# Performance work log

Measured on AMD Instinct MI355X. Metric: run time of the kernel, lower is better.

Reference implementation:

```python
import jax, jax.numpy as jnp
import numpy as np

H = 4096       # hidden_size
NH = 32        # num attention heads
DN = 128       # qk_nope_head_dim
DR = 64        # qk_rope_head_dim
DV = 128       # v_head_dim
QL = 1536      # q_lora_rank
KL = 512       # kv_lora_rank
INH = 32       # indexer heads
IHD = 128      # indexer head_dim (== fp8 quant block -> one scale per head)
TOPK = 512     # index_topk
T = 1024       # prefill tokens
SCALING = (DN + DR) ** -0.5
FP8_MAX = 448.0  # e4m3 max


def _rms(x, w, eps=1e-6):
    return x * jax.lax.rsqrt(jnp.mean(x * x, -1, keepdims=True) + eps) * w


def _ln(x, w, b, eps=1e-6):
    m = jnp.mean(x, -1, keepdims=True)
    v = jnp.mean(jnp.square(x - m), -1, keepdims=True)
    return (x - m) * jax.lax.rsqrt(v + eps) * w + b


def _rope(x, pos):
    # interleaved (non-neox) rotary embedding on the last dim
    d = x.shape[-1]
    inv = 1.0 / (10000.0 ** (jnp.arange(0, d, 2, dtype=jnp.float32) / d))
    ang = pos.astype(jnp.float32)[:, None] * inv  # [T, d/2]
    shape = (x.shape[0],) + (1,) * (x.ndim - 2) + (d // 2,)
    cos = jnp.cos(ang).reshape(shape)
    sin = jnp.sin(ang).reshape(shape)
    x1, x2 = x[..., 0::2], x[..., 1::2]
    return jnp.stack([x1 * cos - x2 * sin, x1 * sin + x2 * cos], -1).reshape(x.shape)


def _forward(hidden_states, w_qkv_a, q_a_ln_w, w_q_b, kv_a_ln_w, w_kv_b, w_o,
             w_idx_qb, w_idx_k, idx_k_ln_w, idx_k_ln_b, w_idx_weights, positions):
    Tq = hidden_states.shape[0]
    neg = jnp.finfo(jnp.float32).min
    # --- fused low-rank QKV-a projection ---
    qkv_a = hidden_states @ w_qkv_a                       # [T, QL+KL+DR]
    q_c, kv_c, k_pe = qkv_a[:, :QL], qkv_a[:, QL:QL + KL], qkv_a[:, QL + KL:]
    q_cn = _rms(q_c, q_a_ln_w)                            # qr (normed q latent)
    # --- MLA decompression ---
    q = (q_cn @ w_q_b).reshape(Tq, NH, DN + DR)
    q_nope, q_pe = q[..., :DN], q[..., DN:]
    kv = (_rms(kv_c, kv_a_ln_w) @ w_kv_b).reshape(Tq, NH, DN + DV)
    k_nope, v = kv[..., :DN], kv[..., DN:]
    q_pe = _rope(q_pe, positions)
    k_pe = _rope(k_pe, positions)                         # [T, DR], shared across heads (MQA)
    # --- lightning indexer (fp8 ue8m0 per-token-group quant emulated in fp32) ---
    qi = (q_cn @ w_idx_qb).reshape(Tq, INH, IHD)
    qi = jnp.concatenate([_rope(qi[..., :DR], positions), qi[..., DR:]], -1)
    ki = _ln(hidden_states @ w_idx_k, idx_k_ln_w, idx_k_ln_b)   # [T, IHD]
    ki = jnp.concatenate([_rope(ki[:, :DR], positions), ki[:, DR:]], -1)
    amax = jnp.max(jnp.abs(qi), -1, keepdims=True)        # group == head (IHD == block 128)
    q_scale = jnp.exp2(jnp.ceil(jnp.log2(jnp.maximum(amax, 1e-10) / FP8_MAX)))  # ue8m0
    qi_q = qi / q_scale                                   # values in fp8 range
    wts = (hidden_states @ w_idx_weights) * q_scale[..., 0]
    wts = wts * (IHD ** -0.5) * (INH ** -0.5)             # [T, INH]
    sim = jax.nn.relu(jnp.einsum('qhd,kd->hqk', qi_q, ki))
    logits = jnp.einsum('qh,hqk->qk', wts, sim)           # [Tq, Tk]
    idx = jnp.arange(Tq)
    causal = idx[:, None] >= idx[None, :]
    logits = jnp.where(causal, logits, neg)
    _, topk_idx = jax.lax.top_k(logits, TOPK)             # [T, TOPK]
    sparse_mask = jnp.zeros((Tq, Tq), bool).at[idx[:, None], topk_idx].set(True) & causal
    # --- sparse MLA attention ---
    qf = jnp.concatenate([q_nope, q_pe], -1)              # [T, NH, DN+DR]
    kf = jnp.concatenate([k_nope, jnp.broadcast_to(k_pe[:, None, :], (Tq, NH, DR))], -1)
    scores = jnp.einsum('qhd,khd->hqk', qf, kf) * SCALING
    scores = jnp.where(sparse_mask[None], scores, neg)
    attn = jax.nn.softmax(scores, -1)
    out = jnp.einsum('hqk,khd->qhd', attn, v).reshape(Tq, NH * DV)
    return out @ w_o                                      # [T, H]


def setup_inputs() -> dict:
    key = jax.random.key(0)
    ks = jax.random.split(key, 8)
    s = 0.02
    return {
        'hidden_states': jax.random.normal(ks[0], (T, H), jnp.float32),
        'positions': jnp.arange(T, dtype=jnp.int32),
        'w_qkv_a': jax.random.normal(ks[1], (H, QL + KL + DR), jnp.float32) * s,
        'q_a_ln_w': jnp.ones((QL,), jnp.float32),
        'w_q_b': jax.random.normal(ks[2], (QL, NH * (DN + DR)), jnp.float32) * s,
        'kv_a_ln_w': jnp.ones((KL,), jnp.float32),
        'w_kv_b': jax.random.normal(ks[3], (KL, NH * (DN + DV)), jnp.float32) * s,
        'w_o': jax.random.normal(ks[4], (NH * DV, H), jnp.float32) * s,
        'w_idx_qb': jax.random.normal(ks[5], (QL, INH * IHD), jnp.float32) * s,
        'w_idx_k': jax.random.normal(ks[6], (H, IHD), jnp.float32) * s,
        'idx_k_ln_w': jnp.ones((IHD,), jnp.float32),
        'idx_k_ln_b': jnp.zeros((IHD,), jnp.float32),
        'w_idx_weights': jax.random.normal(ks[7], (H, INH), jnp.float32) * s,
    }


def reference(hidden_states, positions, w_qkv_a, q_a_ln_w, w_q_b, kv_a_ln_w, w_kv_b, w_o,
              w_idx_qb, w_idx_k, idx_k_ln_w, idx_k_ln_b, w_idx_weights):
    return _forward(hidden_states, w_qkv_a, q_a_ln_w, w_q_b, kv_a_ln_w, w_kv_b, w_o,
                    w_idx_qb, w_idx_k, idx_k_ln_w, idx_k_ln_b, w_idx_weights, positions)
```

## Files before the change

### kernel.cpp

```cpp
#include <hip/hip_runtime.h>
#include <hip/hip_bf16.h>
#include <math.h>
#include <type_traits>

#define TT   1024
#define HH   4096
#define NHH  32
#define DNN  128
#define DRR  64
#define DVV  128
#define QLL  1536
#define KLL  512
#define INHH 32
#define IHDD 128
#define TOPKK 512
#define QKVN 2112

typedef __attribute__((ext_vector_type(8))) short short8;
typedef __attribute__((ext_vector_type(4))) short short4v;
typedef __attribute__((ext_vector_type(4))) float f32x4;

static __device__ __constant__ float kScaling = 0.07216878364870322f;
static __device__ __constant__ float kWtsScale = 0.015625f;

static __device__ __forceinline__ short f2bf(float f) {
  unsigned u = __float_as_uint(f);
  unsigned r = (u + 0x7fffu + ((u >> 16) & 1u)) >> 16;
  return (short)r;
}
static __device__ __forceinline__ float bf2f(short s) {
  return __uint_as_float(((unsigned)(unsigned short)s) << 16);
}
static __device__ __forceinline__ void gl16(const void* g, void* l) {
  __builtin_amdgcn_global_load_lds(
      (const __attribute__((address_space(1))) unsigned int*)g,
      (__attribute__((address_space(3))) unsigned int*)l, 16, 0, 0);
}
static __device__ __forceinline__ int xcd_swz(int n, int nwg) {
  const int q = nwg >> 3, r = nwg & 7;
  const int x = n & 7, i = n >> 3;
  return (x < r ? x * (q + 1) : r * (q + 1) + (x - r) * q) + i;
}

template <typename CT>
__global__ __launch_bounds__(256) void gemm_bf16(const short* __restrict__ A,
                                                 const short* __restrict__ Bt,
                                                 CT* __restrict__ C,
                                                 int M, int N, int K) {
  __shared__ short As[64 * 64];
  __shared__ short Bs[128 * 64];
  int flat = blockIdx.x + gridDim.x * blockIdx.y;
  flat = xcd_swz(flat, gridDim.x * gridDim.y);
  const int byg = flat % gridDim.y;
  const int bxg = flat / gridDim.y;
  const int tid = threadIdx.x;
  const int lane = tid & 63, wv = tid >> 6;
  const int wc = wv * 32;
  const int bm = byg * 64, bn = bxg * 128;
  const int l15 = lane & 15, l4 = lane >> 4;
  const int sx = (l15 & 7) * 8;
  f32x4 acc[4][2];
#pragma unroll
  for (int i = 0; i < 4; ++i)
#pragma unroll
    for (int j = 0; j < 2; ++j) acc[i][j] = f32x4{0.f, 0.f, 0.f, 0.f};
  for (int k0 = 0; k0 < K; k0 += 64) {
    __syncthreads();
#pragma unroll
    for (int i = 0; i < 2; ++i) {
      const int idx = tid + i * 256;
      const int row = idx >> 3, c8 = (idx & 7) * 8;
      const int cs = c8 ^ ((row & 7) * 8);
      gl16(A + (size_t)(bm + row) * K + k0 + cs, &As[idx * 8]);
    }
#pragma unroll
    for (int i = 0; i < 4; ++i) {
      const int idx = tid + i * 256;
      const int row = idx >> 3, c8 = (idx & 7) * 8;
      const int cs = c8 ^ ((row & 7) * 8);
      gl16(Bt + (size_t)(bn + row) * K + k0 + cs, &Bs[idx * 8]);
    }
    __syncthreads();
    short8 fa[4][2], fb[2][2];
#pragma unroll
    for (int rt = 0; rt < 4; ++rt)
#pragma unroll
      for (int kk = 0; kk < 2; ++kk)
        fa[rt][kk] = *(const short8*)(&As[(rt * 16 + l15) * 64 + ((kk * 32 + l4 * 8) ^ sx)]);
#pragma unroll
    for (int ct = 0; ct < 2; ++ct)
#pragma unroll
      for (int kk = 0; kk < 2; ++kk)
        fb[ct][kk] = *(const short8*)(&Bs[(wc + ct * 16 + l15) * 64 + ((kk * 32 + l4 * 8) ^ sx)]);
#pragma unroll
    for (int kk = 0; kk < 2; ++kk)
#pragma unroll
      for (int rt = 0; rt < 4; ++rt)
#pragma unroll
        for (int ct = 0; ct < 2; ++ct)
          acc[rt][ct] = __builtin_amdgcn_mfma_f32_16x16x32_bf16(fa[rt][kk], fb[ct][kk], acc[rt][ct], 0, 0, 0);
  }
#pragma unroll
  for (int rt = 0; rt < 4; ++rt)
#pragma unroll
    for (int ct = 0; ct < 2; ++ct)
#pragma unroll
      for (int r = 0; r < 4; ++r) {
        const int row = bm + rt * 16 + l4 * 4 + r;
        const int col = bn + wc + ct * 16 + l15;
        const float v = acc[rt][ct][r];
        if constexpr (std::is_same<CT, float>::value) C[(size_t)row * N + col] = v;
        else C[(size_t)row * N + col] = __float2bfloat16(v);
      }
}

__global__ __launch_bounds__(256) void gemm1_splitk(const short* __restrict__ A,
                                                    const short* __restrict__ Bt,
                                                    float* __restrict__ part,
                                                    int M, int Np, int K, int kchunk) {
  __shared__ short As[64 * 64];
  __shared__ short Bs[128 * 64];
  int flat = blockIdx.x + gridDim.x * (blockIdx.y + gridDim.y * blockIdx.z);
  flat = xcd_swz(flat, gridDim.x * gridDim.y * gridDim.z);
  const int byg = flat % gridDim.y;
  int tmp = flat / gridDim.y;
  const int bxg = tmp % gridDim.x, bzg = tmp / gridDim.x;
  const int tid = threadIdx.x;
  const int lane = tid & 63, wv = tid >> 6;
  const int wc = wv * 32;
  const int bm = byg * 64, bn = bxg * 128;
  const int kbeg = bzg * kchunk;
  const int l15 = lane & 15, l4 = lane >> 4;
  const int sx = (l15 & 7) * 8;
  f32x4 acc[4][2];
#pragma unroll
  for (int i = 0; i < 4; ++i)
#pragma unroll
    for (int j = 0; j < 2; ++j) acc[i][j] = f32x4{0.f, 0.f, 0.f, 0.f};
  for (int k0 = kbeg; k0 < kbeg + kchunk; k0 += 64) {
    __syncthreads();
#pragma unroll
    for (int i = 0; i < 2; ++i) {
      const int idx = tid + i * 256;
      const int row = idx >> 3, c8 = (idx & 7) * 8;
      const int cs = c8 ^ ((row & 7) * 8);
      gl16(A + (size_t)(bm + row) * K + k0 + cs, &As[idx * 8]);
    }
#pragma unroll
    for (int i = 0; i < 4; ++i) {
      const int idx = tid + i * 256;
      const int row = idx >> 3, c8 = (idx & 7) * 8;
      const int cs = c8 ^ ((row & 7) * 8);
      gl16(Bt + (size_t)(bn + row) * K + k0 + cs, &Bs[idx * 8]);
    }
    __syncthreads();
    short8 fa[4][2], fb[2][2];
#pragma unroll
    for (int rt = 0; rt < 4; ++rt)
#pragma unroll
      for (int kk = 0; kk < 2; ++kk)
        fa[rt][kk] = *(const short8*)(&As[(rt * 16 + l15) * 64 + ((kk * 32 + l4 * 8) ^ sx)]);
#pragma unroll
    for (int ct = 0; ct < 2; ++ct)
#pragma unroll
      for (int kk = 0; kk < 2; ++kk)
        fb[ct][kk] = *(const short8*)(&Bs[(wc + ct * 16 + l15) * 64 + ((kk * 32 + l4 * 8) ^ sx)]);
#pragma unroll
    for (int kk = 0; kk < 2; ++kk)
#pragma unroll
      for (int rt = 0; rt < 4; ++rt)
#pragma unroll
        for (int ct = 0; ct < 2; ++ct)
          acc[rt][ct] = __builtin_amdgcn_mfma_f32_16x16x32_bf16(fa[rt][kk], fb[ct][kk], acc[rt][ct], 0, 0, 0);
  }
  float* dst = part + (size_t)bzg * M * Np;
#pragma unroll
  for (int rt = 0; rt < 4; ++rt)
#pragma unroll
    for (int ct = 0; ct < 2; ++ct)
#pragma unroll
      for (int r = 0; r < 4; ++r)
        dst[(size_t)(bm + rt * 16 + l4 * 4 + r) * Np + bn + wc + ct * 16 + l15] =
            acc[rt][ct][r];
}

__global__ __launch_bounds__(256) void gemm3(const short* __restrict__ Ah,
                                             const short* __restrict__ Al,
                                             const short* __restrict__ Bth,
                                             const short* __restrict__ Btl,
                                             float* __restrict__ part,
                                             int M, int Np, int K, int kchunk) {
  __shared__ short AS[64 * 64], BS[128 * 64];
  int flat = blockIdx.x + gridDim.x * (blockIdx.y + gridDim.y * blockIdx.z);
  flat = xcd_swz(flat, gridDim.x * gridDim.y * gridDim.z);
  const int byg = flat % gridDim.y;
  int tmp = flat / gridDim.y;
  const int bxg = tmp % gridDim.x, bzg = tmp / gridDim.x;
  const int tid = threadIdx.x;
  const int lane = tid & 63, wv = tid >> 6;
  const int wc = wv * 32;
  const int l15 = lane & 15, l4 = lane >> 4;
  const int sx = (l15 & 7) * 8;
  const int bm = byg * 64, bn = bxg * 128;
  const int kbeg = bzg * kchunk;
  f32x4 acc[4][2];
#pragma unroll
  for (int i = 0; i < 4; ++i)
#pragma unroll
    for (int j = 0; j < 2; ++j) acc[i][j] = f32x4{0.f, 0.f, 0.f, 0.f};
  for (int k0 = kbeg; k0 < kbeg + kchunk; k0 += 32) {
    __syncthreads();
#pragma unroll
    for (int i = 0; i < 2; ++i) {
      const int idx = tid + i * 256;
      const int row = idx >> 3, c8 = (idx & 7) * 8;
      const int cs = c8 ^ ((row & 7) * 8);
      const short* srcA = (cs < 32) ? (Ah + (size_t)(bm + row) * K + k0 + cs)
                                    : (Al + (size_t)(bm + row) * K + k0 + (cs - 32));
      gl16(srcA, &AS[idx * 8]);
    }
#pragma unroll
    for (int i = 0; i < 4; ++i) {
      const int idx = tid + i * 256;
      const int row = idx >> 3, c8 = (idx & 7) * 8;
      const int cs = c8 ^ ((row & 7) * 8);
      const short* srcB = (cs < 32) ? (Bth + (size_t)(bn + row) * K + k0 + cs)
                                    : (Btl + (size_t)(bn + row) * K + k0 + (cs - 32));
      gl16(srcB, &BS[idx * 8]);
    }
    __syncthreads();
    short8 fah[4], fal[4], fbh[2], fbl[2];
#pragma unroll
    for (int rt = 0; rt < 4; ++rt) {
      const int row = rt * 16 + l15;
      fah[rt] = *(const short8*)&AS[row * 64 + ((l4 * 8) ^ sx)];
      fal[rt] = *(const short8*)&AS[row * 64 + ((32 + l4 * 8) ^ sx)];
    }
#pragma unroll
    for (int ct = 0; ct < 2; ++ct) {
      const int row = wc + ct * 16 + l15;
      fbh[ct] = *(const short8*)&BS[row * 64 + ((l4 * 8) ^ sx)];
      fbl[ct] = *(const short8*)&BS[row * 64 + ((32 + l4 * 8) ^ sx)];
    }
#pragma unroll
    for (int ct = 0; ct < 2; ++ct)
#pragma unroll
      for (int rt = 0; rt < 4; ++rt) {
        acc[rt][ct] = __builtin_amdgcn_mfma_f32_16x16x32_bf16(fah[rt], fbh[ct], acc[rt][ct], 0, 0, 0);
        acc[rt][ct] = __builtin_amdgcn_mfma_f32_16x16x32_bf16(fah[rt], fbl[ct], acc[rt][ct], 0, 0, 0);
        acc[rt][ct] = __builtin_amdgcn_mfma_f32_16x16x32_bf16(fal[rt], fbh[ct], acc[rt][ct], 0, 0, 0);
      }
  }
  float* dst = part + (size_t)bzg * M * Np;
#pragma unroll
  for (int rt = 0; rt < 4; ++rt)
#pragma unroll
    for (int ct = 0; ct < 2; ++ct)
#pragma unroll
      for (int r = 0; r < 4; ++r)
        dst[(size_t)(bm + rt * 16 + l4 * 4 + r) * Np + bn + wc + ct * 16 + l15] =
            acc[rt][ct][r];
}

__global__ __launch_bounds__(256) void reduce_splitk(const float* __restrict__ part,
                                                     float* __restrict__ C,
                                                     int M, int Np, int Nout, int ldC,
                                                     int ksplit) {
  const int c = blockIdx.x * 256 + threadIdx.x;
  const int m = blockIdx.y;
  if (c >= Nout) return;
  float s = 0.f;
  for (int z = 0; z < ksplit; ++z) s += part[((size_t)z * M + m) * Np + c];
  C[(size_t)m * ldC + c] = s;
}

__global__ __launch_bounds__(256) void qkv_post(const float* __restrict__ qpart,
                                                const float* __restrict__ tpart,
                                                const float* __restrict__ q_ln_w,
                                                const float* __restrict__ kv_ln_w,
                                                const int* __restrict__ pos,
                                                short* __restrict__ qcn_bf,
                                                short* __restrict__ qcn_lo,
                                                short* __restrict__ kvn_bf,
                                                short* __restrict__ kpe_bf) {
  const int t = blockIdx.x, tid = threadIdx.x;
  __shared__ float red[4];
  float qv[6];
  float ss = 0.f;
#pragma unroll
  for (int j = 0; j < 6; ++j) {
    const int c = tid + j * 256;
    float s = 0.f;
#pragma unroll
    for (int z = 0; z < 4; ++z) s += qpart[((size_t)z * TT + t) * QLL + c];
    qv[j] = s;
    ss = fmaf(s, s, ss);
  }
#pragma unroll
  for (int o = 32; o > 0; o >>= 1) ss += __shfl_xor(ss, o);
  if ((tid & 63) == 0) red[tid >> 6] = ss;
  __syncthreads();
  const float rq = rsqrtf((red[0] + red[1] + red[2] + red[3]) / (float)QLL + 1e-6f);
  __syncthreads();
#pragma unroll
  for (int j = 0; j < 6; ++j) {
    const int c = tid + j * 256;
    const float v = qv[j] * rq * q_ln_w[c];
    const short h = f2bf(v);
    qcn_bf[(size_t)t * QLL + c] = h;
    qcn_lo[(size_t)t * QLL + c] = f2bf(v - bf2f(h));
  }
  float kv2[2];
  float ss2 = 0.f;
#pragma unroll
  for (int j = 0; j < 2; ++j) {
    const int c = tid + j * 256;
    float s = 0.f;
#pragma unroll
    for (int z = 0; z < 4; ++z) s += tpart[((size_t)z * TT + t) * 640 + c];
    kv2[j] = s;
    ss2 = fmaf(s, s, ss2);
  }
#pragma unroll
  for (int o = 32; o > 0; o >>= 1) ss2 += __shfl_xor(ss2, o);
  if ((tid & 63) == 0) red[tid >> 6] = ss2;
  __syncthreads();
  const float rkv = rsqrtf((red[0] + red[1] + red[2] + red[3]) / (float)KLL + 1e-6f);
#pragma unroll
  for (int j = 0; j < 2; ++j) {
    const int c = tid + j * 256;
    kvn_bf[(size_t)t * KLL + c] = f2bf(kv2[j] * rkv * kv_ln_w[c]);
  }
  if (tid < 32) {
    float x1 = 0.f, x2 = 0.f;
#pragma unroll
    for (int z = 0; z < 4; ++z) {
      x1 += tpart[((size_t)z * TT + t) * 640 + 512 + 2 * tid];
      x2 += tpart[((size_t)z * TT + t) * 640 + 512 + 2 * tid + 1];
    }
    const float inv = powf(10000.f, -(float)tid * (1.f / 32.f));
    float sn, cs;
    sincosf((float)pos[t] * inv, &sn, &cs);
    kpe_bf[(size_t)t * 64 + 2 * tid]     = f2bf(x1 * cs - x2 * sn);
    kpe_bf[(size_t)t * 64 + 2 * tid + 1] = f2bf(x1 * sn + x2 * cs);
  }
}

__global__ __launch_bounds__(256) void ki_prep2(const float* __restrict__ part,
                                                const float* __restrict__ w,
                                                const float* __restrict__ b,
                                                const int* __restrict__ pos,
                                                short* __restrict__ kih,
                                                short* __restrict__ kil,
                                                float* __restrict__ wtsb) {
  const int t = blockIdx.x, tid = threadIdx.x;
  __shared__ float red[4], red2[4];
  float s = 0.f;
#pragma unroll
  for (int z = 0; z < 8; ++z) s += part[((size_t)z * TT + t) * 256 + tid];
  if (tid >= 128 && tid < 160) wtsb[(size_t)t * 32 + (tid - 128)] = s;
  const float v = (tid < 128) ? s : 0.f;
  float sm = v;
#pragma unroll
  for (int o = 32; o > 0; o >>= 1) sm += __shfl_xor(sm, o);
  if ((tid & 63) == 0) red[tid >> 6] = sm;
  __syncthreads();
  const float m = (red[0] + red[1]) * (1.f / 128.f);
  const float dv = v - m;
  float sq = (tid < 128) ? dv * dv : 0.f;
#pragma unroll
  for (int o = 32; o > 0; o >>= 1) sq += __shfl_xor(sq, o);
  if ((tid & 63) == 0) red2[tid >> 6] = sq;
  __syncthreads();
  const float var = (red2[0] + red2[1]) * (1.f / 128.f);
  if (tid < 128) {
    float x = dv * rsqrtf(var + 1e-6f) * w[tid] + b[tid];
    if (tid < 64) {
      const float part2 = __shfl_xor(x, 1);
      const int pi = tid >> 1;
      const float inv = powf(10000.f, -(float)pi * (1.f / 32.f));
      float sn, cs;
      sincosf((float)pos[t] * inv, &sn, &cs);
      x = (tid & 1) ? (part2 * sn + x * cs) : (x * cs - part2 * sn);
    }
    const short h = f2bf(x);
    kih[(size_t)t * 128 + tid] = h;
    kil[(size_t)t * 128 + tid] = f2bf(x - bf2f(h));
  }
}

__global__ __launch_bounds__(256) void split_cast(const float* __restrict__ in,
                                                  short* __restrict__ hi,
                                                  short* __restrict__ lo, int n4) {
  const int i = blockIdx.x * 256 + threadIdx.x;
  if (i >= n4) return;
  float4 v = *(const float4*)(in + (size_t)i * 4);
  float av[4] = {v.x, v.y, v.z, v.w};
  short4v h, l;
#pragma unroll
  for (int e = 0; e < 4; ++e) {
    h[e] = f2bf(av[e]);
    l[e] = f2bf(av[e] - bf2f(h[e]));
  }
  *(short4v*)(hi + (size_t)i * 4) = h;
  *(short4v*)(lo + (size_t)i * 4) = l;
}

__global__ __launch_bounds__(256) void transpose_cast_g(const float* __restrict__ B,
                                                        short* __restrict__ Bt,
                                                        int K, int ldB, int col0, int Ncols) {
  __shared__ float tile[64][65];
  const int tid = threadIdx.x;
  const int k0 = blockIdx.y * 64, n0 = blockIdx.x * 64;
  const int nl = tid >> 3, kc = (tid & 7) * 8;
  if (n0 >= Ncols) {
    short8 z = {0, 0, 0, 0, 0, 0, 0, 0};
#pragma unroll
    for (int i = 0; i < 2; ++i) {
      const int n = nl + i * 32;
      *(short8*)(Bt + (size_t)(n0 + n) * K + k0 + kc) = z;
    }
    return;
  }
  const int r = tid >> 4, c4 = (tid & 15) * 4;
#pragma unroll
  for (int i = 0; i < 4; ++i) {
    float4 v = *(const float4*)(B + (size_t)(k0 + r + i * 16) * ldB + col0 + n0 + c4);
    tile[r + i * 16][c4 + 0] = v.x;
    tile[r + i * 16][c4 + 1] = v.y;
    tile[r + i * 16][c4 + 2] = v.z;
    tile[r + i * 16][c4 + 3] = v.w;
  }
  __syncthreads();
#pragma unroll
  for (int i = 0; i < 2; ++i) {
    const int n = nl + i * 32;
    short8 o;
#pragma unroll
    for (int e = 0; e < 8; ++e) o[e] = f2bf(tile[kc + e][n]);
    *(short8*)(Bt + (size_t)(n0 + n) * K + k0 + kc) = o;
  }
}

__global__ __launch_bounds__(256) void transpose_split_cast(const float* __restrict__ B,
                                                            short* __restrict__ Bth,
                                                            short* __restrict__ Btl,
                                                            int K, int ldB, int col0,
                                                            int Ncols) {
  __shared__ float tile[64][65];
  const int tid = threadIdx.x;
  const int k0 = blockIdx.y * 64, n0 = blockIdx.x * 64;
  const int nl = tid >> 3, kc = (tid & 7) * 8;
  if (n0 >= Ncols) {
    short8 z = {0, 0, 0, 0, 0, 0, 0, 0};
#pragma unroll
    for (int i = 0; i < 2; ++i) {
      const int n = nl + i * 32;
      *(short8*)(Bth + (size_t)(n0 + n) * K + k0 + kc) = z;
      *(short8*)(Btl + (size_t)(n0 + n) * K + k0 + kc) = z;
    }
    return;
  }
  const int r = tid >> 4, c4 = (tid & 15) * 4;
#pragma unroll
  for (int i = 0; i < 4; ++i) {
    float4 v = make_float4(0.f, 0.f, 0.f, 0.f);
    if (n0 + c4 < Ncols)
      v = *(const float4*)(B + (size_t)(k0 + r + i * 16) * ldB + col0 + n0 + c4);
    tile[r + i * 16][c4 + 0] = v.x;
    tile[r + i * 16][c4 + 1] = v.y;
    tile[r + i * 16][c4 + 2] = v.z;
    tile[r + i * 16][c4 + 3] = v.w;
  }
  __syncthreads();
#pragma unroll
  for (int i = 0; i < 2; ++i) {
    const int n = nl + i * 32;
    short8 oh, ol;
#pragma unroll
    for (int e = 0; e < 8; ++e) {
      const float x = tile[kc + e][n];
      oh[e] = f2bf(x);
      ol[e] = f2bf(x - bf2f(oh[e]));
    }
    *(short8*)(Bth + (size_t)(n0 + n) * K + k0 + kc) = oh;
    *(short8*)(Btl + (size_t)(n0 + n) * K + k0 + kc) = ol;
  }
}

__global__ void q_rope_repack(const short* __restrict__ qbuf,
                              short* __restrict__ qhout,
                              const int* __restrict__ pos) {
  const int q = blockIdx.x, h = blockIdx.y;
  const int p = threadIdx.x;
  const short* s = qbuf + ((size_t)q * 32 + h) * 192;
  short* d = qhout + ((size_t)h * 1024 + q) * 192;
  float x1 = bf2f(s[2 * p]), x2 = bf2f(s[2 * p + 1]);
  if (p >= 64) {
    const int i = p - 64;
    const float inv = powf(10000.f, -(float)i * (1.f / 32.f));
    const float ang = (float)pos[q] * inv;
    float sn, cs;
    sincosf(ang, &sn, &cs);
    const float a = x1 * cs - x2 * sn, b = x1 * sn + x2 * cs;
    x1 = a; x2 = b;
  }
  d[2 * p]     = f2bf(x1);
  d[2 * p + 1] = f2bf(x2);
}

__global__ __launch_bounds__(256) void qi_rope_repack_split(const float* __restrict__ qib,
                                                            const int* __restrict__ pos,
                                                            short* __restrict__ qhh,
                                                            short* __restrict__ qhl) {
  const int qt = blockIdx.x, h = blockIdx.y;
  const int tid = threadIdx.x;
#pragma unroll
  for (int i = 0; i < 8; ++i) {
    const int idx = tid + i * 256;
    const int q = idx >> 5, c = idx & 31;
    float4 v = *(const float4*)(qib + ((size_t)(qt * 64 + q) * 32 + h) * 128 + c * 4);
    float av[4] = {v.x, v.y, v.z, v.w};
    if (c < 16) {
      const int qg = qt * 64 + q;
      const float p = (float)pos[qg];
      float sn0, cs0, sn1, cs1;
      sincosf(p * powf(10000.f, -(float)(c * 2) * (1.f / 32.f)), &sn0, &cs0);
      sincosf(p * powf(10000.f, -(float)(c * 2 + 1) * (1.f / 32.f)), &sn1, &cs1);
      const float a0 = av[0] * cs0 - av[1] * sn0, a1 = av[0] * sn0 + av[1] * cs0;
      const float a2 = av[2] * cs1 - av[3] * sn1, a3 = av[2] * sn1 + av[3] * cs1;
      av[0] = a0; av[1] = a1; av[2] = a2; av[3] = a3;
    }
    short4v hv, lv;
#pragma unroll
    for (int e = 0; e < 4; ++e) {
      hv[e] = f2bf(av[e]);
      lv[e] = f2bf(av[e] - bf2f(hv[e]));
    }
    const size_t off = ((size_t)h * 1024 + qt * 64 + q) * 128 + c * 4;
    *(short4v*)(qhh + off) = hv;
    *(short4v*)(qhl + off) = lv;
  }
}

__global__ __launch_bounds__(256) void kv_repack(const short* __restrict__ kvb,
                                                 const short* __restrict__ kpe,
                                                 short* __restrict__ kfout,
                                                 short* __restrict__ vtout) {
  const int kt = blockIdx.x, h = blockIdx.y;
  const int tid = threadIdx.x;
  const int k0 = kt * 64;
  __shared__ short vtile[64][136];
#pragma unroll
  for (int i = 0; i < 6; ++i) {
    const int idx = tid + i * 256;
    const int row = idx / 24, c = idx - row * 24;
    short8 v = (c < 16) ? *(const short8*)(kvb + ((size_t)(k0 + row) * 32 + h) * 256 + c * 8)
                        : *(const short8*)(kpe + (size_t)(k0 + row) * 64 + (c - 16) * 8);
    *(short8*)(kfout + ((size_t)h * 1024 + k0 + row) * 192 + c * 8) = v;
  }
#pragma unroll
  for (int i = 0; i < 4; ++i) {
    const int idx = tid + i * 256;
    const int row = idx >> 4, c = idx & 15;
    *(short8*)&vtile[row][c * 8] =
        *(const short8*)(kvb + ((size_t)(k0 + row) * 32 + h) * 256 + 128 + c * 8);
  }
  __syncthreads();
#pragma unroll
  for (int i = 0; i < 4; ++i) {
    const int idx = tid + i * 256;
    const int d = idx >> 3, kc = idx & 7;
    short8 o;
#pragma unroll
    for (int e = 0; e < 8; ++e) o[e] = vtile[kc * 8 + e][d];
    *(short8*)(vtout + ((size_t)h * 128 + d) * 1024 + k0 + kc * 8) = o;
  }
}

__global__ __launch_bounds__(256) void logits_mfma(const short* __restrict__ qih,
                                                   const short* __restrict__ qil,
                                                   const short* __restrict__ kih_g,
                                                   const short* __restrict__ kil_g,
                                                   const float* __restrict__ wts,
                                                   float* __restrict__ part) {
  const int bid = xcd_swz(blockIdx.x, gridDim.x);
  int bq = (int)((sqrtf(8.f * bid + 1.f) - 1.f) * 0.5f);
  while ((bq + 1) * (bq + 2) / 2 <= bid) ++bq;
  while (bq * (bq + 1) / 2 > bid) --bq;
  const int bk = bid - bq * (bq + 1) / 2;
  const int g = blockIdx.y;
  __shared__ short kih[64 * 128], kil[64 * 128];
  __shared__ float swts[64][8];
  const int tid = threadIdx.x;
  const int lane = tid & 63, wv = tid >> 6;
  const int wr = (wv >> 1) * 32, wc = (wv & 1) * 32;
  const int l15 = lane & 15, l4 = lane >> 4;
  const int q0 = bq * 64, k0 = bk * 64;
  {
    const int r0 = tid >> 4;
    const int c8 = (tid & 15) * 8;
#pragma unroll
    for (int i = 0; i < 4; ++i) {
      const int row = r0 + i * 16;
      gl16(kih_g + (size_t)(k0 + row) * 128 + c8, &kih[(tid + i * 256) * 8]);
      gl16(kil_g + (size_t)(k0 + row) * 128 + c8, &kil[(tid + i * 256) * 8]);
    }
  }
#pragma unroll
  for (int i = 0; i < 2; ++i) {
    const int idx = tid + i * 256;
    swts[idx >> 3][idx & 7] = wts[(size_t)(q0 + (idx >> 3)) * 32 + g * 8 + (idx & 7)];
  }
  __syncthreads();
  short8 kbh[2][4], kbl[2][4];
#pragma unroll
  for (int ct = 0; ct < 2; ++ct)
#pragma unroll
    for (int ks = 0; ks < 4; ++ks) {
      kbh[ct][ks] = *(const short8*)&kih[(wc + ct * 16 + l15) * 128 + ks * 32 + l4 * 8];
      kbl[ct][ks] = *(const short8*)&kil[(wc + ct * 16 + l15) * 128 + ks * 32 + l4 * 8];
    }
  f32x4 lacc[2][2];
#pragma unroll
  for (int i = 0; i < 2; ++i)
#pragma unroll
    for (int j = 0; j < 2; ++j) lacc[i][j] = f32x4{0.f, 0.f, 0.f, 0.f};
  for (int hh = 0; hh < 8; ++hh) {
    const int h = g * 8 + hh;
    short8 qah[2][4], qal[2][4];
#pragma unroll
    for (int rt = 0; rt < 2; ++rt)
#pragma unroll
      for (int ks = 0; ks < 4; ++ks) {
        const size_t off = ((size_t)h * 1024 + q0 + wr + rt * 16 + l15) * 128 + ks * 32 + l4 * 8;
        qah[rt][ks] = *(const short8*)(qih + off);
        qal[rt][ks] = *(const short8*)(qil + off);
      }
    f32x4 hacc[2][2];
#pragma unroll
    for (int i = 0; i < 2; ++i)
#pragma unroll
      for (int j = 0; j < 2; ++j) hacc[i][j] = f32x4{0.f, 0.f, 0.f, 0.f};
#pragma unroll
    for (int ks = 0; ks < 4; ++ks)
#pragma unroll
      for (int rt = 0; rt < 2; ++rt)
#pragma unroll
        for (int ct = 0; ct < 2; ++ct) {
          hacc[rt][ct] = __builtin_amdgcn_mfma_f32_16x16x32_bf16(qah[rt][ks], kbh[ct][ks], hacc[rt][ct], 0, 0, 0);
          hacc[rt][ct] = __builtin_amdgcn_mfma_f32_16x16x32_bf16(qah[rt][ks], kbl[ct][ks], hacc[rt][ct], 0, 0, 0);
          hacc[rt][ct] = __builtin_amdgcn_mfma_f32_16x16x32_bf16(qal[rt][ks], kbh[ct][ks], hacc[rt][ct], 0, 0, 0);
        }
#pragma unroll
    for (int rt = 0; rt < 2; ++rt)
#pragma unroll
      for (int ct = 0; ct < 2; ++ct)
#pragma unroll
        for (int r = 0; r < 4; ++r) {
          const int row = wr + rt * 16 + l4 * 4 + r;
          const float w = swts[row][hh] * kWtsScale;
          lacc[rt][ct][r] = fmaf(w, fmaxf(hacc[rt][ct][r], 0.f), lacc[rt][ct][r]);
        }
  }
#pragma unroll
  for (int rt = 0; rt < 2; ++rt)
#pragma unroll
    for (int ct = 0; ct < 2; ++ct)
#pragma unroll
      for (int r = 0; r < 4; ++r)
        part[(size_t)g * TT * TT + (size_t)(q0 + wr + rt * 16 + l4 * 4 + r) * TT +
             (k0 + wc + ct * 16 + l15)] = lacc[rt][ct][r];
}

__global__ __launch_bounds__(256) void topk_mask(const float* __restrict__ part,
                                                 unsigned* __restrict__ maskbuf) {
  const int w = threadIdx.x >> 6;
  const int lane = threadIdx.x & 63;
  const int q = blockIdx.x * 4 + w;
  const size_t NN = (size_t)TT * TT;
  __shared__ unsigned long long bl[4][16];
  unsigned v[16];
#pragma unroll
  for (int j = 0; j < 16; ++j) {
    const int k = j * 64 + lane;
    unsigned uv = 0u;
    if (k <= q) {
      const size_t o = (size_t)q * TT + k;
      const float s = part[o] + part[NN + o] + part[2 * NN + o] + part[3 * NN + o];
      unsigned bb = __float_as_uint(s);
      uv = (bb & 0x80000000u) ? ~bb : (bb | 0x80000000u);
    }
    v[j] = uv;
  }
  if (q + 1 <= TOPKK) {
#pragma unroll
    for (int j = 0; j < 16; ++j) {
      const unsigned long long m = __ballot(j * 64 + lane <= q);
      if (lane == 0) bl[w][j] = m;
    }
  } else {
    unsigned lo = 1u, hi = 0xFFFFFFFFu;
    while (lo < hi) {
      const unsigned mid = lo + ((hi - lo) >> 1) + ((hi - lo) & 1u);
      int c = 0;
#pragma unroll
      for (int j = 0; j < 16; ++j) c += __popcll(__ballot(v[j] >= mid));
      if (c >= TOPKK) lo = mid; else hi = mid - 1u;
    }
    const unsigned ustar = lo;
    int nGreater = 0;
#pragma unroll
    for (int j = 0; j < 16; ++j) nGreater += __popcll(__ballot(v[j] > ustar));
    int need = TOPKK - nGreater;
    const unsigned long long lanemask = lane ? (~0ull >> (64 - lane)) : 0ull;
#pragma unroll
    for (int j = 0; j < 16; ++j) {
      const unsigned long long bg = __ballot(v[j] > ustar);
      const unsigned long long be = __ballot(v[j] == ustar);
      const int ce = __popcll(be);
      const int take = need < ce ? need : ce;
      const int rank = __popcll(be & lanemask);
      const bool selme = ((be >> lane) & 1ull) && (rank < take);
      const unsigned long long m = bg | __ballot(selme);
      if (lane == 0) bl[w][j] = m;
      need -= take;
    }
  }
  __builtin_amdgcn_s_waitcnt(0);
  if (lane < 32)
    maskbuf[(size_t)q * 32 + lane] = (unsigned)(bl[w][lane >> 1] >> ((lane & 1) * 32));
}

__global__ __launch_bounds__(256) void attn_mfma(const short* __restrict__ qh,
                                                 const short* __restrict__ kf,
                                                 const short* __restrict__ vt,
                                                 const unsigned* __restrict__ maskbuf,
                                                 short* __restrict__ ao) {
  const int h = blockIdx.x;
  const int yy = blockIdx.y;
  const int qt = (yy < 8) ? (yy * 2) : (31 - yy * 2);
  const int tid = threadIdx.x;
  const int lane = tid & 63, w = tid >> 6;
  const int l15 = lane & 15, l4 = lane >> 4;
  const int q0 = qt * 64;
  __shared__ short kfs[64 * 200];
  __shared__ short vts[128 * 72];
  __shared__ short ps[4][16][72];
  __shared__ unsigned m32s[64][2];
  short8 qf[6];
#pragma unroll
  for (int ks = 0; ks < 6; ++ks)
    qf[ks] = *(const short8*)(qh + ((size_t)h * 1024 + q0 + w * 16 + l15) * 192 + ks * 32 + l4 * 8);
  f32x4 of[8];
#pragma unroll
  for (int dt = 0; dt < 8; ++dt) of[dt] = f32x4{0.f, 0.f, 0.f, 0.f};
  float m[4], l[4];
#pragma unroll
  for (int r = 0; r < 4; ++r) { m[r] = -INFINITY; l[r] = 0.f; }

  for (int kt = 0; kt <= qt; ++kt) {
    const int k0 = kt * 64;
    __syncthreads();
#pragma unroll
    for (int i = 0; i < 6; ++i) {
      const int idx = tid + i * 256;
      const int row = idx / 24, c = idx - row * 24;
      *(short8*)&kfs[row * 200 + c * 8] =
          *(const short8*)(kf + ((size_t)h * 1024 + k0 + row) * 192 + c * 8);
    }
#pragma unroll
    for (int i = 0; i < 4; ++i) {
      const int idx = tid + i * 256;
      const int row = idx >> 3, c = idx & 7;
      *(short8*)&vts[row * 72 + c * 8] =
          *(const short8*)(vt + ((size_t)h * 128 + row) * 1024 + k0 + c * 8);
    }
    if (tid < 128)
      m32s[tid >> 1][tid & 1] = maskbuf[(size_t)(q0 + (tid >> 1)) * 32 + (k0 >> 5) + (tid & 1)];
    __syncthreads();
    f32x4 sacc[4];
#pragma unroll
    for (int j = 0; j < 4; ++j) sacc[j] = f32x4{0.f, 0.f, 0.f, 0.f};
#pragma unroll
    for (int ks = 0; ks < 6; ++ks)
#pragma unroll
      for (int j = 0; j < 4; ++j) {
        short8 kb = *(const short8*)&kfs[(j * 16 + l15) * 200 + ks * 32 + l4 * 8];
        sacc[j] = __builtin_amdgcn_mfma_f32_16x16x32_bf16(qf[ks], kb, sacc[j], 0, 0, 0);
      }
    float tmax[4] = {-INFINITY, -INFINITY, -INFINITY, -INFINITY};
#pragma unroll
    for (int j = 0; j < 4; ++j)
#pragma unroll
      for (int r = 0; r < 4; ++r) {
        const int kcol = j * 16 + l15;
        const unsigned um = m32s[w * 16 + l4 * 4 + r][kcol >> 5];
        float s = sacc[j][r] * kScaling;
        s = ((um >> (kcol & 31)) & 1u) ? s : -INFINITY;
        sacc[j][r] = s;
        tmax[r] = fmaxf(tmax[r], s);
      }
#pragma unroll
    for (int r = 0; r < 4; ++r) {
      tmax[r] = fmaxf(tmax[r], __shfl_xor(tmax[r], 1));
      tmax[r] = fmaxf(tmax[r], __shfl_xor(tmax[r], 2));
      tmax[r] = fmaxf(tmax[r], __shfl_xor(tmax[r], 4));
      tmax[r] = fmaxf(tmax[r], __shfl_xor(tmax[r], 8));
    }
    float f[4];
#pragma unroll
    for (int r = 0; r < 4; ++r) {
      const float mn = fmaxf(m[r], tmax[r]);
      f[r] = __expf(fmaxf(m[r], -1e30f) - fmaxf(mn, -1e30f));
      m[r] = mn;
      l[r] *= f[r];
    }
    float psum[4] = {0.f, 0.f, 0.f, 0.f};
#pragma unroll
    for (int j = 0; j < 4; ++j)
#pragma unroll
      for (int r = 0; r < 4; ++r) {
        const float p = __expf(sacc[j][r] - fmaxf(m[r], -1e30f));
        psum[r] += p;
        ps[w][l4 * 4 + r][j * 16 + l15] = f2bf(p);
      }
#pragma unroll
    for (int r = 0; r < 4; ++r) {
      psum[r] += __shfl_xor(psum[r], 1);
      psum[r] += __shfl_xor(psum[r], 2);
      psum[r] += __shfl_xor(psum[r], 4);
      psum[r] += __shfl_xor(psum[r], 8);
      l[r] += psum[r];
    }
#pragma unroll
    for (int dt = 0; dt < 8; ++dt)
#pragma unroll
      for (int r = 0; r < 4; ++r) of[dt][r] *= f[r];
    short8 pa0 = *(const short8*)&ps[w][l15][l4 * 8];
    short8 pa1 = *(const short8*)&ps[w][l15][32 + l4 * 8];
#pragma unroll
    for (int dt = 0; dt < 8; ++dt) {
      short8 vb0 = *(const short8*)&vts[(dt * 16 + l15) * 72 + l4 * 8];
      short8 vb1 = *(const short8*)&vts[(dt * 16 + l15) * 72 + 32 + l4 * 8];
      of[dt] = __builtin_amdgcn_mfma_f32_16x16x32_bf16(pa0, vb0, of[dt], 0, 0, 0);
      of[dt] = __builtin_amdgcn_mfma_f32_16x16x32_bf16(pa1, vb1, of[dt], 0, 0, 0);
    }
  }
#pragma unroll
  for (int r = 0; r < 4; ++r) {
    const float invl = 1.f / l[r];
#pragma unroll
    for (int dt = 0; dt < 8; ++dt)
      ao[(size_t)(q0 + w * 16 + l4 * 4 + r) * 4096 + h * 128 + dt * 16 + l15] =
          f2bf(of[dt][r] * invl);
  }
}

extern "C" void kernel_launch(void* const* d_in, const int* in_sizes, int n_in,
                              void* d_out, int out_size, void* d_ws, size_t ws_size,
                              hipStream_t stream) {
  const float* hidden     = (const float*)d_in[0];
  const int*   positions  = (const int*)d_in[1];
  const float* w_qkv_a    = (const float*)d_in[2];
  const float* q_a_ln_w   = (const float*)d_in[3];
  const float* w_q_b      = (const float*)d_in[4];
  const float* kv_a_ln_w  = (const float*)d_in[5];
  const float* w_kv_b     = (const float*)d_in[6];
  const float* w_o        = (const float*)d_in[7];
  const float* w_idx_qb   = (const float*)d_in[8];
  const float* w_idx_k    = (const float*)d_in[9];
  const float* idx_k_ln_w = (const float*)d_in[10];
  const float* idx_k_ln_b = (const float*)d_in[11];
  const float* w_idx_w    = (const float*)d_in[12];
  float* out = (float*)d_out;

  float* ws = (float*)d_ws;
  size_t off = 0;
  auto take = [&](size_t n) { float* p = ws + off; off += n; return p; };
  short* qcn_bf  = (short*)take((size_t)TT * QLL / 2);
  short* qcn_lo  = (short*)take((size_t)TT * QLL / 2);
  short* kvn_bf  = (short*)take((size_t)TT * KLL / 2);
  short* qbuf    = (short*)take((size_t)TT * NHH * 192 / 2);
  short* kvbuf   = (short*)take((size_t)TT * NHH * 256 / 2);
  short* kpe_bf  = (short*)take((size_t)TT * 32);
  float* qib     = take((size_t)TT * INHH * IHDD);
  float* wtsb    = take((size_t)TT * INHH);
  short* kih_g   = (short*)take((size_t)TT * IHDD / 2);
  short* kil_g   = (short*)take((size_t)TT * IHDD / 2);
  short* qhb     = (short*)take((size_t)NHH * TT * 192 / 2);
  short* qih_h   = (short*)take((size_t)INHH * TT * 128 / 2);
  short* qih_l   = (short*)take((size_t)INHH * TT * 128 / 2);
  short* kfb     = (short*)take((size_t)NHH * TT * 192 / 2);
  short* vtb     = (short*)take((size_t)NHH * 128 * TT / 2);
  float* part4   = take((size_t)4 * TT * TT);
  unsigned* maskbuf = (unsigned*)take((size_t)TT * 32);
  short* hid_h   = (short*)take((size_t)TT * HH / 2);
  short* hid_l   = (short*)take((size_t)TT * HH / 2);
  short* wqkva_h = (short*)take((size_t)QLL * HH / 2);
  short* wqkva_l = (short*)take((size_t)QLL * HH / 2);
  short* wtail_t = (short*)take((size_t)640 * HH / 2);
  short* wsk_h   = (short*)take((size_t)256 * HH / 2);
  short* wsk_l   = (short*)take((size_t)256 * HH / 2);
  short* widxqb_h = (short*)take((size_t)HH * QLL / 2);
  short* widxqb_l = (short*)take((size_t)HH * QLL / 2);
  short* wqb_t   = (short*)take((size_t)6144 * QLL / 2);
  short* wkvb_t  = (short*)take((size_t)8192 * KLL / 2);
  short* ao   = (short*)part4;
  short* wo_t = hid_h;
  float* skpart = part4;
  float* qkvpart = (float*)vtb;
  float* tailpart = (float*)kvbuf;
  float* idxpart = (float*)qhb;

  const dim3 blk(256);
  split_cast<<<dim3(TT * HH / 4 / 256), blk, 0, stream>>>(hidden, hid_h, hid_l, TT * HH / 4);
  transpose_split_cast<<<dim3(QLL / 64, HH / 64), blk, 0, stream>>>(w_qkv_a, wqkva_h, wqkva_l, HH, QKVN, 0, QLL);
  transpose_cast_g<<<dim3(640 / 64, HH / 64), blk, 0, stream>>>(w_qkv_a, wtail_t, HH, QKVN, QLL, QKVN - QLL);
  transpose_split_cast<<<dim3(HH / 64, QLL / 64), blk, 0, stream>>>(w_idx_qb, widxqb_h, widxqb_l, QLL, HH, 0, HH);
  transpose_split_cast<<<dim3(2, HH / 64), blk, 0, stream>>>(w_idx_k, wsk_h, wsk_l, HH, 128, 0, 128);
  transpose_split_cast<<<dim3(2, HH / 64), blk, 0, stream>>>(w_idx_w, wsk_h + (size_t)128 * HH,
                                                            wsk_l + (size_t)128 * HH, HH, 32, 0, 32);
  transpose_cast_g<<<dim3(6144 / 64, QLL / 64), blk, 0, stream>>>(w_q_b, wqb_t, QLL, 6144, 0, 6144);
  transpose_cast_g<<<dim3(8192 / 64, KLL / 64), blk, 0, stream>>>(w_kv_b, wkvb_t, KLL, 8192, 0, 8192);
  gemm3<<<dim3(2, 16, 8), blk, 0, stream>>>(hid_h, hid_l, wsk_h, wsk_l,
                                            skpart, TT, 256, HH, HH / 8);
  ki_prep2<<<dim3(TT), blk, 0, stream>>>(skpart, idx_k_ln_w, idx_k_ln_b, positions,
                                         kih_g, kil_g, wtsb);
  gemm3<<<dim3(QLL / 128, 16, 4), blk, 0, stream>>>(hid_h, hid_l, wqkva_h, wqkva_l,
                                                    qkvpart, TT, QLL, HH, HH / 4);
  gemm1_splitk<<<dim3(5, 16, 4), blk, 0, stream>>>(hid_h, wtail_t, tailpart, TT, 640, HH, HH / 4);
  qkv_post<<<dim3(TT), blk, 0, stream>>>(qkvpart, tailpart, q_a_ln_w, kv_a_ln_w, positions,
                                         qcn_bf, qcn_lo, kvn_bf, kpe_bf);
  transpose_cast_g<<<dim3(HH / 64, HH / 64), blk, 0, stream>>>(w_o, wo_t, HH, HH, 0, HH);
  gemm3<<<dim3(HH / 128, 16, 2), blk, 0, stream>>>(qcn_bf, qcn_lo, widxqb_h, widxqb_l,
                                                   idxpart, TT, HH, QLL, QLL / 2);
  reduce_splitk<<<dim3(HH / 256, TT), blk, 0, stream>>>(idxpart, qib, TT, HH, HH, HH, 2);
  gemm_bf16<__hip_bfloat16><<<dim3(48, 16), blk, 0, stream>>>(qcn_bf, wqb_t, (__hip_bfloat16*)qbuf, TT, 6144, QLL);
  gemm_bf16<__hip_bfloat16><<<dim3(64, 16), blk, 0, stream>>>(kvn_bf, wkvb_t, (__hip_bfloat16*)kvbuf, TT, 8192, KLL);
  q_rope_repack<<<dim3(TT, NHH), 96, 0, stream>>>(qbuf, qhb, positions);
  qi_rope_repack_split<<<dim3(16, INHH), blk, 0, stream>>>(qib, positions, qih_h, qih_l);
  kv_repack<<<dim3(16, NHH), blk, 0, stream>>>(kvbuf, kpe_bf, kfb, vtb);
  logits_mfma<<<dim3(136, 4), blk, 0, stream>>>(qih_h, qih_l, kih_g, kil_g, wtsb, part4);
  topk_mask<<<dim3(TT / 4), blk, 0, stream>>>(part4, maskbuf);
  attn_mfma<<<dim3(NHH, 16), blk, 0, stream>>>(qhb, kfb, vtb, maskbuf, ao);
  gemm_bf16<float><<<dim3(32, 16), blk, 0, stream>>>(ao, wo_t, out, TT, HH, NHH * DVV);
}
```

Baseline: 506.6 us.

## Fuse RoPE/repack epilogues into q_b and kv_b GEMMs and drop split-K reduce

Adds a q_b GEMM whose epilogue applies rotary embedding and writes the head-major attention query layout directly. It also adds a kv_b GEMM whose epilogue writes K in head-major layout and V transposed via shared memory. The qi RoPE repack now sums the two split-K partial planes itself, so the separate reduce kernel and intermediate buffers are gone. This removes several full round trips through global memory and some launches. In exchange the GEMM epilogues do per-element powf/sincos and narrow scattered stores, and a small kpe_fill kernel is added.

```diff
diff --git a/kernel.cpp b/kernel.cpp
--- a/kernel.cpp
+++ b/kernel.cpp
@@ -112,6 +112,182 @@
         if constexpr (std::is_same<CT, float>::value) C[(size_t)row * N + col] = v;
         else C[(size_t)row * N + col] = __float2bfloat16(v);
       }
+}
+
+__global__ __launch_bounds__(256) void gemm_qb(const short* __restrict__ A,
+                                               const short* __restrict__ Bt,
+                                               const int* __restrict__ pos,
+                                               short* __restrict__ qhb) {
+  const int M = TT, N = 6144, K = QLL;
+  __shared__ short As[64 * 64];
+  __shared__ short Bs[128 * 64];
+  int flat = blockIdx.x + gridDim.x * blockIdx.y;
+  flat = xcd_swz(flat, gridDim.x * gridDim.y);
+  const int byg = flat % gridDim.y;
+  const int bxg = flat / gridDim.y;
+  const int tid = threadIdx.x;
+  const int lane = tid & 63, wv = tid >> 6;
+  const int wc = wv * 32;
+  const int bm = byg * 64, bn = bxg * 128;
+  const int l15 = lane & 15, l4 = lane >> 4;
+  const int sx = (l15 & 7) * 8;
+  f32x4 acc[4][2];
+#pragma unroll
+  for (int i = 0; i < 4; ++i)
+#pragma unroll
+    for (int j = 0; j < 2; ++j) acc[i][j] = f32x4{0.f, 0.f, 0.f, 0.f};
+  for (int k0 = 0; k0 < K; k0 += 64) {
+    __syncthreads();
+#pragma unroll
+    for (int i = 0; i < 2; ++i) {
+      const int idx = tid + i * 256;
+      const int row = idx >> 3, c8 = (idx & 7) * 8;
+      const int cs = c8 ^ ((row & 7) * 8);
+      gl16(A + (size_t)(bm + row) * K + k0 + cs, &As[idx * 8]);
+    }
+#pragma unroll
+    for (int i = 0; i < 4; ++i) {
+      const int idx = tid + i * 256;
+      const int row = idx >> 3, c8 = (idx & 7) * 8;
+      const int cs = c8 ^ ((row & 7) * 8);
+      gl16(Bt + (size_t)(bn + row) * K + k0 + cs, &Bs[idx * 8]);
+    }
+    __syncthreads();
+    short8 fa[4][2], fb[2][2];
+#pragma unroll
+    for (int rt = 0; rt < 4; ++rt)
+#pragma unroll
+      for (int kk = 0; kk < 2; ++kk)
+        fa[rt][kk] = *(const short8*)(&As[(rt * 16 + l15) * 64 + ((kk * 32 + l4 * 8) ^ sx)]);
+#pragma unroll
+    for (int ct = 0; ct < 2; ++ct)
+#pragma unroll
+      for (int kk = 0; kk < 2; ++kk)
+        fb[ct][kk] = *(const short8*)(&Bs[(wc + ct * 16 + l15) * 64 + ((kk * 32 + l4 * 8) ^ sx)]);
+#pragma unroll
+    for (int kk = 0; kk < 2; ++kk)
+#pragma unroll
+      for (int rt = 0; rt < 4; ++rt)
+#pragma unroll
+        for (int ct = 0; ct < 2; ++ct)
+          acc[rt][ct] = __builtin_amdgcn_mfma_f32_16x16x32_bf16(fa[rt][kk], fb[ct][kk], acc[rt][ct], 0, 0, 0);
+  }
+#pragma unroll
+  for (int rt = 0; rt < 4; ++rt)
+#pragma unroll
+    for (int r = 0; r < 4; ++r) {
+      const int row = bm + rt * 16 + l4 * 4 + r;
+      const float p = (float)pos[row];
+#pragma unroll
+      for (int ct = 0; ct < 2; ++ct) {
+        const int col = bn + wc + ct * 16 + l15;
+        float v = acc[rt][ct][r];
+        const float pv = __shfl_xor(v, 1);
+        const int head = col / 192, d = col - head * 192;
+        if (d >= 128) {
+          const int i = (d - 128) >> 1;
+          const float inv = powf(10000.f, -(float)i * (1.f / 32.f));
+          float sn, cs;
+          sincosf(p * inv, &sn, &cs);
+          v = (col & 1) ? (pv * sn + v * cs) : (v * cs - pv * sn);
+        }
+        qhb[((size_t)head * 1024 + row) * 192 + d] = f2bf(v);
+      }
+    }
+}
+
+__global__ __launch_bounds__(256) void gemm_kvb(const short* __restrict__ A,
+                                                const short* __restrict__ Bt,
+                                                short* __restrict__ kfb,
+                                                short* __restrict__ vtb) {
+  const int K = KLL;
+  __shared__ short As[64 * 64];
+  __shared__ short Bs[128 * 64];
+  __shared__ short tr[128 * 66];
+  int flat = blockIdx.x + gridDim.x * blockIdx.y;
+  flat = xcd_swz(flat, gridDim.x * gridDim.y);
+  const int byg = flat % gridDim.y;
+  const int bxg = flat / gridDim.y;
+  const int tid = threadIdx.x;
+  const int lane = tid & 63, wv = tid >> 6;
+  const int wc = wv * 32;
+  const int bm = byg * 64, bn = bxg * 128;
+  const int l15 = lane & 15, l4 = lane >> 4;
+  const int sx = (l15 & 7) * 8;
+  f32x4 acc[4][2];
+#pragma unroll
+  for (int i = 0; i < 4; ++i)
+#pragma unroll
+    for (int j = 0; j < 2; ++j) acc[i][j] = f32x4{0.f, 0.f, 0.f, 0.f};
+  for (int k0 = 0; k0 < K; k0 += 64) {
+    __syncthreads();
+#pragma unroll
+    for (int i = 0; i < 2; ++i) {
+      const int idx = tid + i * 256;
+      const int row = idx >> 3, c8 = (idx & 7) * 8;
+      const int cs = c8 ^ ((row & 7) * 8);
+      gl16(A + (size_t)(bm + row) * K + k0 + cs, &As[idx * 8]);
+    }
+#pragma unroll
+    for (int i = 0; i < 4; ++i) {
+      const int idx = tid + i * 256;
+      const int row = idx >> 3, c8 = (idx & 7) * 8;
+      const int cs = c8 ^ ((row & 7) * 8);
+      gl16(Bt + (size_t)(bn + row) * K + k0 + cs, &Bs[idx * 8]);
+    }
+    __syncthreads();
+    short8 fa[4][2], fb[2][2];
+#pragma unroll
+    for (int rt = 0; rt < 4; ++rt)
+#pragma unroll
+      for (int kk = 0; kk < 2; ++kk)
+        fa[rt][kk] = *(const short8*)(&As[(rt * 16 + l15) * 64 + ((kk * 32 + l4 * 8) ^ sx)]);
+#pragma unroll
+    for (int ct = 0; ct < 2; ++ct)
+#pragma unroll
+      for (int kk = 0; kk < 2; ++kk)
+        fb[ct][kk] = *(const short8*)(&Bs[(wc + ct * 16 + l15) * 64 + ((kk * 32 + l4 * 8) ^ sx)]);
+#pragma unroll
+    for (int kk = 0; kk < 2; ++kk)
+#pragma unroll
+      for (int rt = 0; rt < 4; ++rt)
+#pragma unroll
+        for (int ct = 0; ct < 2; ++ct)
+          acc[rt][ct] = __builtin_amdgcn_mfma_f32_16x16x32_bf16(fa[rt][kk], fb[ct][kk], acc[rt][ct], 0, 0, 0);
+  }
+  const int h = bn >> 8;
+  const bool isv = (bn >> 7) & 1;
+  if (!isv) {
+#pragma unroll
+    for (int rt = 0; rt < 4; ++rt)
+#pragma unroll
+      for (int ct = 0; ct < 2; ++ct)
+#pragma unroll
+        for (int r = 0; r < 4; ++r) {
+          const int row = bm + rt * 16 + l4 * 4 + r;
+          const int d = wc + ct * 16 + l15;
+          kfb[((size_t)h * 1024 + row) * 192 + d] = f2bf(acc[rt][ct][r]);
+        }
+  } else {
+    __syncthreads();
+#pragma unroll
+    for (int rt = 0; rt < 4; ++rt)
+#pragma unroll
+      for (int ct = 0; ct < 2; ++ct)
+#pragma unroll
+        for (int r = 0; r < 4; ++r)
+          tr[(wc + ct * 16 + l15) * 66 + rt * 16 + l4 * 4 + r] = f2bf(acc[rt][ct][r]);
+    __syncthreads();
+    const int d = tid >> 1, half = tid & 1;
+    short* dst = vtb + ((size_t)h * 128 + d) * 1024 + bm + half * 32;
+#pragma unroll
+    for (int c = 0; c < 4; ++c) {
+      short8 o;
+#pragma unroll
+      for (int e = 0; e < 8; ++e) o[e] = tr[d * 66 + half * 32 + c * 8 + e];
+      *(short8*)(dst + c * 8) = o;
+    }
+  }
 }
 
 __global__ __launch_bounds__(256) void gemm1_splitk(const short* __restrict__ A,
@@ -262,18 +438,6 @@
             acc[rt][ct][r];
 }
 
-__global__ __launch_bounds__(256) void reduce_splitk(const float* __restrict__ part,
-                                                     float* __restrict__ C,
-                                                     int M, int Np, int Nout, int ldC,
-                                                     int ksplit) {
-  const int c = blockIdx.x * 256 + threadIdx.x;
-  const int m = blockIdx.y;
-  if (c >= Nout) return;
-  float s = 0.f;
-  for (int z = 0; z < ksplit; ++z) s += part[((size_t)z * M + m) * Np + c];
-  C[(size_t)m * ldC + c] = s;
-}
-
 __global__ __launch_bounds__(256) void qkv_post(const float* __restrict__ qpart,
                                                 const float* __restrict__ tpart,
                                                 const float* __restrict__ q_ln_w,
@@ -346,6 +510,14 @@
   }
 }
 
+__global__ __launch_bounds__(256) void kpe_fill(const short* __restrict__ kpe_bf,
+                                                short* __restrict__ kfb) {
+  const int idx = blockIdx.x * 256 + threadIdx.x;
+  const int c = idx & 7, k = (idx >> 3) & 1023, h = idx >> 13;
+  short8 v = *(const short8*)(kpe_bf + k * 64 + c * 8);
+  *(short8*)(kfb + ((size_t)h * 1024 + k) * 192 + 128 + c * 8) = v;
+}
+
 __global__ __launch_bounds__(256) void ki_prep2(const float* __restrict__ part,
                                                 const float* __restrict__ w,
                                                 const float* __restrict__ b,
@@ -488,41 +660,23 @@
   }
 }
 
-__global__ void q_rope_repack(const short* __restrict__ qbuf,
-                              short* __restrict__ qhout,
-                              const int* __restrict__ pos) {
-  const int q = blockIdx.x, h = blockIdx.y;
-  const int p = threadIdx.x;
-  const short* s = qbuf + ((size_t)q * 32 + h) * 192;
-  short* d = qhout + ((size_t)h * 1024 + q) * 192;
-  float x1 = bf2f(s[2 * p]), x2 = bf2f(s[2 * p + 1]);
-  if (p >= 64) {
-    const int i = p - 64;
-    const float inv = powf(10000.f, -(float)i * (1.f / 32.f));
-    const float ang = (float)pos[q] * inv;
-    float sn, cs;
-    sincosf(ang, &sn, &cs);
-    const float a = x1 * cs - x2 * sn, b = x1 * sn + x2 * cs;
-    x1 = a; x2 = b;
-  }
-  d[2 * p]     = f2bf(x1);
-  d[2 * p + 1] = f2bf(x2);
-}
-
-__global__ __launch_bounds__(256) void qi_rope_repack_split(const float* __restrict__ qib,
+__global__ __launch_bounds__(256) void qi_rope_repack_split(const float* __restrict__ idxpart,
                                                             const int* __restrict__ pos,
                                                             short* __restrict__ qhh,
                                                             short* __restrict__ qhl) {
   const int qt = blockIdx.x, h = blockIdx.y;
   const int tid = threadIdx.x;
+  const size_t plane = (size_t)TT * HH;
 #pragma unroll
   for (int i = 0; i < 8; ++i) {
     const int idx = tid + i * 256;
     const int q = idx >> 5, c = idx & 31;
-    float4 v = *(const float4*)(qib + ((size_t)(qt * 64 + q) * 32 + h) * 128 + c * 4);
-    float av[4] = {v.x, v.y, v.z, v.w};
+    const int qg = qt * 64 + q;
+    const size_t base = (size_t)qg * HH + h * 128 + c * 4;
+    float4 v0 = *(const float4*)(idxpart + base);
+    float4 v1 = *(const float4*)(idxpart + plane + base);
+    float av[4] = {v0.x + v1.x, v0.y + v1.y, v0.z + v1.z, v0.w + v1.w};
     if (c < 16) {
-      const int qg = qt * 64 + q;
       const float p = (float)pos[qg];
       float sn0, cs0, sn1, cs1;
       sincosf(p * powf(10000.f, -(float)(c * 2) * (1.f / 32.f)), &sn0, &cs0);
@@ -540,41 +694,6 @@
     const size_t off = ((size_t)h * 1024 + qt * 64 + q) * 128 + c * 4;
     *(short4v*)(qhh + off) = hv;
     *(short4v*)(qhl + off) = lv;
-  }
-}
-
-__global__ __launch_bounds__(256) void kv_repack(const short* __restrict__ kvb,
-                                                 const short* __restrict__ kpe,
-                                                 short* __restrict__ kfout,
-                                                 short* __restrict__ vtout) {
-  const int kt = blockIdx.x, h = blockIdx.y;
-  const int tid = threadIdx.x;
-  const int k0 = kt * 64;
-  __shared__ short vtile[64][136];
-#pragma unroll
-  for (int i = 0; i < 6; ++i) {
-    const int idx = tid + i * 256;
-    const int row = idx / 24, c = idx - row * 24;
-    short8 v = (c < 16) ? *(const short8*)(kvb + ((size_t)(k0 + row) * 32 + h) * 256 + c * 8)
-                        : *(const short8*)(kpe + (size_t)(k0 + row) * 64 + (c - 16) * 8);
-    *(short8*)(kfout + ((size_t)h * 1024 + k0 + row) * 192 + c * 8) = v;
-  }
-#pragma unroll
-  for (int i = 0; i < 4; ++i) {
-    const int idx = tid + i * 256;
-    const int row = idx >> 4, c = idx & 15;
-    *(short8*)&vtile[row][c * 8] =
-        *(const short8*)(kvb + ((size_t)(k0 + row) * 32 + h) * 256 + 128 + c * 8);
-  }
-  __syncthreads();
-#pragma unroll
-  for (int i = 0; i < 4; ++i) {
-    const int idx = tid + i * 256;
-    const int d = idx >> 3, kc = idx & 7;
-    short8 o;
-#pragma unroll
-    for (int e = 0; e < 8; ++e) o[e] = vtile[kc * 8 + e][d];
-    *(short8*)(vtout + ((size_t)h * 128 + d) * 1024 + k0 + kc * 8) = o;
   }
 }
 
@@ -881,18 +1000,15 @@
   short* qcn_bf  = (short*)take((size_t)TT * QLL / 2);
   short* qcn_lo  = (short*)take((size_t)TT * QLL / 2);
   short* kvn_bf  = (short*)take((size_t)TT * KLL / 2);
-  short* qbuf    = (short*)take((size_t)TT * NHH * 192 / 2);
-  short* kvbuf   = (short*)take((size_t)TT * NHH * 256 / 2);
   short* kpe_bf  = (short*)take((size_t)TT * 32);
-  float* qib     = take((size_t)TT * INHH * IHDD);
   float* wtsb    = take((size_t)TT * INHH);
   short* kih_g   = (short*)take((size_t)TT * IHDD / 2);
   short* kil_g   = (short*)take((size_t)TT * IHDD / 2);
   short* qhb     = (short*)take((size_t)NHH * TT * 192 / 2);
+  short* kfb     = (short*)take((size_t)NHH * TT * 192 / 2);
+  short* vtb     = (short*)take((size_t)NHH * 128 * TT / 2);
   short* qih_h   = (short*)take((size_t)INHH * TT * 128 / 2);
   short* qih_l   = (short*)take((size_t)INHH * TT * 128 / 2);
-  short* kfb     = (short*)take((size_t)NHH * TT * 192 / 2);
-  short* vtb     = (short*)take((size_t)NHH * 128 * TT / 2);
   float* part4   = take((size_t)4 * TT * TT);
   unsigned* maskbuf = (unsigned*)take((size_t)TT * 32);
   short* hid_h   = (short*)take((size_t)TT * HH / 2);
@@ -910,7 +1026,7 @@
   short* wo_t = hid_h;
   float* skpart = part4;
   float* qkvpart = (float*)vtb;
-  float* tailpart = (float*)kvbuf;
+  float* tailpart = (float*)qhb;
   float* idxpart = (float*)qhb;
 
   const dim3 blk(256);
@@ -935,12 +1051,10 @@
   transpose_cast_g<<<dim3(HH / 64, HH / 64), blk, 0, stream>>>(w_o, wo_t, HH, HH, 0, HH);
   gemm3<<<dim3(HH / 128, 16, 2), blk, 0, stream>>>(qcn_bf, qcn_lo, widxqb_h, widxqb_l,
                                                    idxpart, TT, HH, QLL, QLL / 2);
-  reduce_splitk<<<dim3(HH / 256, TT), blk, 0, stream>>>(idxpart, qib, TT, HH, HH, HH, 2);
-  gemm_bf16<__hip_bfloat16><<<dim3(48, 16), blk, 0, stream>>>(qcn_bf, wqb_t, (__hip_bfloat16*)qbuf, TT, 6144, QLL);
-  gemm_bf16<__hip_bfloat16><<<dim3(64, 16), blk, 0, stream>>>(kvn_bf, wkvb_t, (__hip_bfloat16*)kvbuf, TT, 8192, KLL);
-  q_rope_repack<<<dim3(TT, NHH), 96, 0, stream>>>(qbuf, qhb, positions);
-  qi_rope_repack_split<<<dim3(16, INHH), blk, 0, stream>>>(qib, positions, qih_h, qih_l);
-  kv_repack<<<dim3(16, NHH), blk, 0, stream>>>(kvbuf, kpe_bf, kfb, vtb);
+  qi_rope_repack_split<<<dim3(16, INHH), blk, 0, stream>>>(idxpart, positions, qih_h, qih_l);
+  gemm_qb<<<dim3(48, 16), blk, 0, stream>>>(qcn_bf, wqb_t, positions, qhb);
+  gemm_kvb<<<dim3(64, 16), blk, 0, stream>>>(kvn_bf, wkvb_t, kfb, vtb);
+  kpe_fill<<<dim3(1024), blk, 0, stream>>>(kpe_bf, kfb);
   logits_mfma<<<dim3(136, 4), blk, 0, stream>>>(qih_h, qih_l, kih_g, kil_g, wtsb, part4);
   topk_mask<<<dim3(TT / 4), blk, 0, stream>>>(part4, maskbuf);
   attn_mfma<<<dim3(NHH, 16), blk, 0, stream>>>(qhb, kfb, vtb, maskbuf, ao);
```

After: 487.1 us. -3.9%, faster.
